# Performance work log

Measured on AMD Instinct MI355X. Metric: run time of the kernel, lower is better.

Reference implementation:

```python
import jax, jax.numpy as jnp
import numpy as np

B, LQ, D, H, NL, NP, DFF = 8, 1800, 256, 8, 4, 4, 1024
DH = D // H
SHAPES = np.array([[100, 150], [50, 75], [25, 38], [13, 19]], dtype=np.int64)
LIN = int((SHAPES[:, 0] * SHAPES[:, 1]).sum())
QN, QP = -8.0, 7.0  # 4-bit signed LSQ


def lsq(w, alpha):
    """LSQ weight quantization (per-tensor scale, STE round/grad-scale)."""
    g = 1.0 / jnp.sqrt(w.size * QP)
    a = alpha * g + jax.lax.stop_gradient(alpha - alpha * g)  # grad-scaled alpha
    wn = jnp.clip(w / a, QN, QP)
    wq = wn + jax.lax.stop_gradient(jnp.round(wn) - wn)       # round with STE
    return wq * a


def linear_q(x, w, b, a):
    return x @ lsq(w, a).T + b


def layer_norm(x, g, b, eps=1e-5):
    m = x.mean(-1, keepdims=True)
    v = ((x - m) ** 2).mean(-1, keepdims=True)
    return (x - m) / jnp.sqrt(v + eps) * g + b


def setup_inputs():
    key = jax.random.key(0)
    ks = list(jax.random.split(key, 20))

    def nrm(i, shape, s=0.02):
        return jax.random.normal(ks[i], shape, jnp.float32) * s

    def alpha(w):
        return 2.0 * jnp.mean(jnp.abs(w)) / jnp.sqrt(QP)

    qW, kW, vW, oW = nrm(0, (D, D)), nrm(1, (D, D)), nrm(2, (D, D)), nrm(3, (D, D))
    val_W = nrm(4, (D, D))
    off_W = nrm(5, (H * NL * NP * 2, D))
    aw_W = nrm(6, (H * NL * NP, D))
    out_W = nrm(7, (D, D))
    W1, W2 = nrm(8, (DFF, D)), nrm(9, (D, DFF))
    lsi = np.concatenate([[0], np.cumsum(SHAPES[:, 0] * SHAPES[:, 1])[:-1]]).astype(np.int64)
    z = jnp.zeros
    return dict(
        tgt=nrm(10, (B, LQ, D), 1.0),
        query_pos=nrm(11, (B, LQ, D), 1.0),
        reference_points=jax.random.uniform(ks[12], (B, LQ, NL, 2), jnp.float32),
        src=nrm(13, (B, LIN, D), 1.0),
        qW=qW, qb=z(D), kW=kW, kb=z(D), vW=vW, vb=z(D), oW=oW, ob=z(D),
        a_q=alpha(qW), a_k=alpha(kW), a_v=alpha(vW), a_o=alpha(oW),
        val_W=val_W, val_b=z(D), a_val=alpha(val_W),
        off_W=off_W, off_b=z(H * NL * NP * 2),
        aw_W=aw_W, aw_b=z(H * NL * NP),
        out_W=out_W, out_b=z(D), a_out=alpha(out_W),
        W1=W1, b1=z(DFF), a_w1=alpha(W1),
        W2=W2, b2=z(D), a_w2=alpha(W2),
        ln1_g=jnp.ones(D), ln1_b=z(D),
        ln2_g=jnp.ones(D), ln2_b=z(D),
        ln3_g=jnp.ones(D), ln3_b=z(D),
        src_spatial_shapes=jnp.asarray(SHAPES),
        level_start_index=jnp.asarray(lsi),
        src_padding_mask=jnp.zeros((B, LIN), dtype=bool),
    )


def reference(tgt, query_pos, reference_points, src,
              qW, qb, kW, kb, vW, vb, oW, ob, a_q, a_k, a_v, a_o,
              val_W, val_b, a_val, off_W, off_b, aw_W, aw_b, out_W, out_b, a_out,
              W1, b1, a_w1, W2, b2, a_w2,
              ln1_g, ln1_b, ln2_g, ln2_b, ln3_g, ln3_b,
              src_spatial_shapes, level_start_index, src_padding_mask):
    shapes = np.asarray(src_spatial_shapes)  # static spatial shapes per level

    # ---- quantized self-attention (dropout = eval mode, i.e. identity) ----
    qk_in = tgt + query_pos
    q = linear_q(qk_in, qW, qb, a_q).reshape(B, LQ, H, DH)
    k = linear_q(qk_in, kW, kb, a_k).reshape(B, LQ, H, DH)
    v = linear_q(tgt, vW, vb, a_v).reshape(B, LQ, H, DH)
    scores = jnp.einsum('bqhd,bkhd->bhqk', q, k) / jnp.sqrt(jnp.float32(DH))
    p = jax.nn.softmax(scores, axis=-1)
    sa = jnp.einsum('bhqk,bkhd->bqhd', p, v).reshape(B, LQ, D)
    tgt = layer_norm(tgt + linear_q(sa, oW, ob, a_o), ln2_g, ln2_b)

    # ---- quantized multi-scale deformable cross-attention ----
    query = tgt + query_pos
    value = linear_q(src, val_W, val_b, a_val)
    value = jnp.where(src_padding_mask[..., None], 0.0, value)
    value = value.reshape(B, LIN, H, DH)
    offs = (query @ off_W.T + off_b).reshape(B, LQ, H, NL, NP, 2)
    aw = (query @ aw_W.T + aw_b).reshape(B, LQ, H, NL * NP)
    aw = jax.nn.softmax(aw, axis=-1).reshape(B, LQ, H, NL, NP)
    # offset normalizer is (W_l, H_l)
    norm = jnp.asarray(shapes[:, ::-1].astype(np.float32))  # [NL, 2]
    loc = reference_points[:, :, None, :, None, :] + offs / norm[None, None, None, :, None, :]

    bidx = jnp.arange(B)[:, None, None, None]
    hidx = jnp.arange(H)[None, None, :, None]
    acc = jnp.zeros((B, LQ, H, DH), jnp.float32)
    start = 0
    for l in range(NL):
        Hl, Wl = int(shapes[l, 0]), int(shapes[l, 1])
        v_l = jax.lax.dynamic_slice_in_dim(value, start, Hl * Wl, 1).reshape(B, Hl, Wl, H, DH)
        # grid_sample semantics: align_corners=False, zero padding
        x = loc[:, :, :, l, :, 0] * Wl - 0.5  # [B, LQ, H, NP]
        y = loc[:, :, :, l, :, 1] * Hl - 0.5
        x0 = jnp.floor(x); y0 = jnp.floor(y)
        x0i = x0.astype(jnp.int32); y0i = y0.astype(jnp.int32)
        wx1 = x - x0; wy1 = y - y0
        wx0 = 1.0 - wx1; wy0 = 1.0 - wy1

        def gather(yi, xi):
            valid = (yi >= 0) & (yi < Hl) & (xi >= 0) & (xi < Wl)
            yc = jnp.clip(yi, 0, Hl - 1); xc = jnp.clip(xi, 0, Wl - 1)
            g = v_l[bidx, yc, xc, hidx]  # [B, LQ, H, NP, DH]
            return g * valid[..., None]

        samp = (gather(y0i, x0i) * (wy0 * wx0)[..., None]
                + gather(y0i, x0i + 1) * (wy0 * wx1)[..., None]
                + gather(y0i + 1, x0i) * (wy1 * wx0)[..., None]
                + gather(y0i + 1, x0i + 1) * (wy1 * wx1)[..., None])
        acc = acc + (aw[:, :, :, l, :, None] * samp).sum(axis=3)
        start += Hl * Wl

    ca = linear_q(acc.reshape(B, LQ, D), out_W, out_b, a_out)
    tgt = layer_norm(tgt + ca, ln1_g, ln1_b)

    # ---- quantized FFN ----
    t2 = linear_q(jax.nn.relu(linear_q(tgt, W1, b1, a_w1)), W2, b2, a_w2)
    tgt = layer_norm(tgt + t2, ln3_g, ln3_b)
    return tgt
```

## Files before the change

kernel.cpp:

```cpp
#include <hip/hip_runtime.h>
#include <hip/hip_bf16.h>

static constexpr int B_   = 8;
static constexpr int LQ_  = 1800;
static constexpr int D_   = 256;
static constexpr int H_   = 8;
static constexpr int DFF_ = 1024;
static constexpr int LIN_ = 19947;
static constexpr int MQ_  = B_ * LQ_;
static constexpr int NELEM_ = MQ_ * D_;

#define CDIV(a, b) (((a) + (b) - 1) / (b))

typedef unsigned short u16;
typedef unsigned int   u32;
typedef unsigned long long u64;
typedef __attribute__((ext_vector_type(8))) __bf16 bf16x8;
typedef __attribute__((ext_vector_type(4))) float  f32x4;
typedef __attribute__((ext_vector_type(4))) u32    u32x4;

#if __has_builtin(__builtin_amdgcn_exp2f)
#define EXP2(x) __builtin_amdgcn_exp2f(x)
#else
#define EXP2(x) exp2f(x)
#endif

__device__ __forceinline__ u16 f2bf(float f) {
    union { __bf16 h; u16 u; } v; v.h = (__bf16)f; return v.u;
}
__device__ __forceinline__ float bf2f(u16 u) {
    union { u32 u; float f; } v; v.u = ((u32)u) << 16;
    return v.f;
}

__device__ __forceinline__ f32x4 mfma_bf16(bf16x8 a, bf16x8 b, f32x4 c) {
    return __builtin_amdgcn_mfma_f32_16x16x32_bf16(a, b, c, 0, 0, 0);
}

__global__ void k_quant(const float* __restrict__ w, const float* __restrict__ alpha,
                        u16* __restrict__ o, int n) {
    int i = blockIdx.x * blockDim.x + threadIdx.x;
    if (i >= n) return;
    float a = alpha[0];
    float wn = fminf(fmaxf(w[i] / a, -8.f), 7.f);
    o[i] = f2bf(rintf(wn) * a);
}

__global__ void k_cvt(const float* __restrict__ w, u16* __restrict__ o, int n) {
    int i = blockIdx.x * blockDim.x + threadIdx.x;
    if (i < n) o[i] = f2bf(w[i]);
}

__global__ void k_addcvt(const float* __restrict__ a, const float* __restrict__ b,
                         u16* __restrict__ o, int n) {
    int i = blockIdx.x * blockDim.x + threadIdx.x;
    if (i < n) o[i] = f2bf(a[i] + b[i]);
}

__global__ void k_addcvt2(const u16* __restrict__ a, const float* __restrict__ b,
                          u16* __restrict__ o, int n) {
    int i = blockIdx.x * blockDim.x + threadIdx.x;
    if (i < n) o[i] = f2bf(bf2f(a[i]) + b[i]);
}

__device__ __forceinline__ bf16x8 loadx(const u16* p) { return *(const bf16x8*)p; }
__device__ __forceinline__ bf16x8 loadx(const float* p) {
    float4 a = *(const float4*)p;
    float4 b = *(const float4*)(p + 4);
    bf16x8 r;
    r[0] = (__bf16)a.x; r[1] = (__bf16)a.y; r[2] = (__bf16)a.z; r[3] = (__bf16)a.w;
    r[4] = (__bf16)b.x; r[5] = (__bf16)b.y; r[6] = (__bf16)b.z; r[7] = (__bf16)b.w;
    return r;
}
__device__ __forceinline__ void storey(float* p, float v) { *p = v; }
__device__ __forceinline__ void storey(u16* p, float v)   { *p = f2bf(v); }

template <typename XT, typename OT, bool RELU>
__global__ __launch_bounds__(256) void k_gemm(
    const XT* __restrict__ X, const u16* __restrict__ W,
    const float* __restrict__ bias, OT* __restrict__ Y,
    int M, int N, int K)
{
    __shared__ u16 As[128 * 40];
    __shared__ u16 Bs[128 * 40];
    const int tid = threadIdx.x;
    const int wave = tid >> 6, lane = tid & 63;
    const int wr = wave >> 1, wc = wave & 1;
    const int fr = lane & 15, fg = lane >> 4;
    const int bm = blockIdx.x * 128, bn = blockIdx.y * 128;
    const int srow = tid >> 2, sc = (tid & 3) * 8;

    f32x4 acc[4][4];
    #pragma unroll
    for (int m = 0; m < 4; ++m)
        #pragma unroll
        for (int n = 0; n < 4; ++n) acc[m][n] = (f32x4){0.f, 0.f, 0.f, 0.f};

    for (int k0 = 0; k0 < K; k0 += 32) {
        __syncthreads();
        #pragma unroll
        for (int i = 0; i < 2; ++i) {
            int row = srow + i * 64;
            int gr = bm + row; if (gr > M - 1) gr = M - 1;
            bf16x8 xa = loadx(X + (size_t)gr * K + k0 + sc);
            *(bf16x8*)&As[row * 40 + sc] = xa;
            bf16x8 wb = *(const bf16x8*)(W + (size_t)(bn + row) * K + k0 + sc);
            *(bf16x8*)&Bs[row * 40 + sc] = wb;
        }
        __syncthreads();
        bf16x8 af[4], bg[4];
        #pragma unroll
        for (int m = 0; m < 4; ++m)
            af[m] = *(const bf16x8*)&As[(wr * 64 + m * 16 + fr) * 40 + fg * 8];
        #pragma unroll
        for (int n = 0; n < 4; ++n)
            bg[n] = *(const bf16x8*)&Bs[(wc * 64 + n * 16 + fr) * 40 + fg * 8];
        #pragma unroll
        for (int m = 0; m < 4; ++m)
            #pragma unroll
            for (int n = 0; n < 4; ++n)
                acc[m][n] = mfma_bf16(af[m], bg[n], acc[m][n]);
    }

    #pragma unroll
    for (int m = 0; m < 4; ++m) {
        #pragma unroll
        for (int i = 0; i < 4; ++i) {
            int grow = bm + wr * 64 + m * 16 + fg * 4 + i;
            if (grow >= M) continue;
            #pragma unroll
            for (int n = 0; n < 4; ++n) {
                int gcol = bn + wc * 64 + n * 16 + fr;
                float v = acc[m][n][i] + bias[gcol];
                if (RELU) v = fmaxf(v, 0.f);
                storey(Y + (size_t)grow * N + gcol, v);
            }
        }
    }
}

__global__ __launch_bounds__(256) void k_attn(
    const u16* __restrict__ Q, const u16* __restrict__ K,
    const u16* __restrict__ V, u16* __restrict__ O)
{
    __shared__ u16 Ks[128 * 40];
    __shared__ u16 Vt[32 * 136];
    const int b = blockIdx.z, h = blockIdx.y;
    const int q0 = blockIdx.x * 64;
    const int tid = threadIdx.x;
    const int wave = tid >> 6, lane = tid & 63;
    const int fr = lane & 15, fg = lane >> 4;
    constexpr float C2 = 0.25503486f;

    int qg = q0 + wave * 16 + fr; if (qg >= LQ_) qg = LQ_ - 1;
    bf16x8 qf;
    {
        bf16x8 qraw = *(const bf16x8*)&Q[((size_t)(b * LQ_ + qg)) * 256 + h * 32 + fg * 8];
        #pragma unroll
        for (int j = 0; j < 8; ++j) qf[j] = (__bf16)((float)qraw[j] * C2);
    }

    const bf16x8 ones = {(__bf16)1.f, (__bf16)1.f, (__bf16)1.f, (__bf16)1.f,
                         (__bf16)1.f, (__bf16)1.f, (__bf16)1.f, (__bf16)1.f};

    f32x4 o0 = (f32x4){0.f,0.f,0.f,0.f}, o1 = (f32x4){0.f,0.f,0.f,0.f};
    f32x4 lacc = (f32x4){0.f,0.f,0.f,0.f};

    const int kr = tid >> 1, kc = (tid & 1) * 16;
    const int vp = lane, vdh = wave * 8;
    const int cp = ((vp >> 4) << 4) | (((vp >> 1) & 3) << 2) | (((vp >> 3) & 1) << 1) | (vp & 1);

    for (int kb0 = 0; kb0 < LQ_; kb0 += 128) {
        const bool tail = (kb0 + 128 > LQ_);
        __syncthreads();
        {
            int kg = kb0 + kr; if (kg >= LQ_) kg = LQ_ - 1;
            const u16* kp = &K[((size_t)(b * LQ_ + kg)) * 256 + h * 32 + kc];
            *(bf16x8*)&Ks[kr * 40 + kc]     = *(const bf16x8*)kp;
            *(bf16x8*)&Ks[kr * 40 + kc + 8] = *(const bf16x8*)(kp + 8);
            int v0 = kb0 + 2 * vp, v1 = v0 + 1;
            if (v0 >= LQ_) v0 = LQ_ - 1;
            if (v1 >= LQ_) v1 = LQ_ - 1;
            union { bf16x8 v; u16 s[8]; } va, vb2;
            va.v  = *(const bf16x8*)&V[((size_t)(b * LQ_ + v0)) * 256 + h * 32 + vdh];
            vb2.v = *(const bf16x8*)&V[((size_t)(b * LQ_ + v1)) * 256 + h * 32 + vdh];
            #pragma unroll
            for (int j = 0; j < 8; ++j)
                *(u32*)&Vt[(vdh + j) * 136 + 2 * cp] = (u32)va.s[j] | ((u32)vb2.s[j] << 16);
        }
        __syncthreads();

        u32x4 pq[4];
        #pragma unroll
        for (int f = 0; f < 8; ++f) {
            bf16x8 ka = *(const bf16x8*)&Ks[(f * 16 + fr) * 40 + fg * 8];
            f32x4 s = mfma_bf16(ka, qf, (f32x4){0.f,0.f,0.f,0.f});
            if (tail) {
                #pragma unroll
                for (int i = 0; i < 4; ++i)
                    if (kb0 + f * 16 + fg * 4 + i >= LQ_) s[i] = -3e38f;
            }
            float p0 = EXP2(s[0]), p1 = EXP2(s[1]);
            float p2 = EXP2(s[2]), p3 = EXP2(s[3]);
            union { __bf16 h[2]; u32 w; } c0, c1;
            c0.h[0] = (__bf16)p0; c0.h[1] = (__bf16)p1;
            c1.h[0] = (__bf16)p2; c1.h[1] = (__bf16)p3;
            pq[f >> 1][(f & 1) * 2 + 0] = c0.w;
            pq[f >> 1][(f & 1) * 2 + 1] = c1.w;
        }

        #pragma unroll
        for (int ks = 0; ks < 4; ++ks) {
            bf16x8 pb  = __builtin_bit_cast(bf16x8, pq[ks]);
            bf16x8 va0 = *(const bf16x8*)&Vt[fr * 136 + ks * 32 + fg * 8];
            bf16x8 va1 = *(const bf16x8*)&Vt[(16 + fr) * 136 + ks * 32 + fg * 8];
            o0 = mfma_bf16(va0, pb, o0);
            o1 = mfma_bf16(va1, pb, o1);
            lacc = mfma_bf16(ones, pb, lacc);
        }
    }

    float inv = 1.f / lacc[0];
    int qout = q0 + wave * 16 + fr;
    if (qout < LQ_) {
        size_t base = ((size_t)(b * LQ_ + qout)) * 256 + h * 32;
        #pragma unroll
        for (int i = 0; i < 4; ++i) {
            O[base + fg * 4 + i]      = f2bf(o0[i] * inv);
            O[base + 16 + fg * 4 + i] = f2bf(o1[i] * inv);
        }
    }
}

__device__ __forceinline__ float ldf(const float* p) { return *p; }
__device__ __forceinline__ float ldf(const u16* p)   { return bf2f(*p); }

template <typename RT, typename OT>
__global__ __launch_bounds__(256) void k_resln(
    const u16* __restrict__ X, const RT* __restrict__ R,
    const float* __restrict__ g, const float* __restrict__ bb,
    OT* __restrict__ O)
{
    const int row = blockIdx.x;
    const int d = threadIdx.x;
    const size_t off = (size_t)row * D_ + d;
    float v = ldf(R + off) + bf2f(X[off]);
    __shared__ float r1[4], r2[4];
    int lane = d & 63, wid = d >> 6;
    float s = v;
    #pragma unroll
    for (int o_ = 32; o_ >= 1; o_ >>= 1) s += __shfl_xor(s, o_);
    if (lane == 0) r1[wid] = s;
    __syncthreads();
    float mean = (r1[0] + r1[1] + r1[2] + r1[3]) * (1.f / 256.f);
    float dv = v - mean;
    float sq = dv * dv;
    #pragma unroll
    for (int o_ = 32; o_ >= 1; o_ >>= 1) sq += __shfl_xor(sq, o_);
    if (lane == 0) r2[wid] = sq;
    __syncthreads();
    float var = (r2[0] + r2[1] + r2[2] + r2[3]) * (1.f / 256.f);
    storey(O + off, dv / sqrtf(var + 1e-5f) * g[d] + bb[d]);
}

__global__ __launch_bounds__(256) void k_sample(
    const float* __restrict__ offs, const float* __restrict__ aw,
    const u16* __restrict__ value, const float* __restrict__ refp,
    u16* __restrict__ acc_out)
{
    __shared__ u32 pts[2][128][8];
    const int t = threadIdx.x;
    const int bq0 = blockIdx.x * 2;
    const int b = bq0 / LQ_;

    constexpr int Hl[4] = {100, 50, 25, 13};
    constexpr int Wl[4] = {150, 75, 38, 19};
    constexpr int LS[4] = {0, 15000, 18750, 19700};

    {
        const int qsub = t >> 7;
        const int pt = t & 127;
        const int h = pt >> 4, lp = pt & 15;
        const int l = lp >> 2, p = lp & 3;
        const int bq = bq0 + qsub;

        float2 oxy = *(const float2*)&offs[(size_t)bq * 256 + h * 32 + l * 8 + p * 2];
        float av = aw[(size_t)bq * 128 + h * 16 + lp];
        float mx = av;
        #pragma unroll
        for (int s = 1; s < 16; s <<= 1) mx = fmaxf(mx, __shfl_xor(mx, s));
        float e = __expf(av - mx);
        float sum = e;
        #pragma unroll
        for (int s = 1; s < 16; s <<= 1) sum += __shfl_xor(sum, s);
        float a = e / sum;

        float2 rxy = *(const float2*)&refp[(size_t)bq * 8 + l * 2];
        const float Wf = (float)Wl[l], Hf = (float)Hl[l];
        float x = (rxy.x + oxy.x / Wf) * Wf - 0.5f;
        float y = (rxy.y + oxy.y / Hf) * Hf - 0.5f;
        float x0f = floorf(x), y0f = floorf(y);
        int x0 = (int)x0f, y0 = (int)y0f;
        float wx1 = x - x0f, wy1 = y - y0f;
        float wx0 = 1.f - wx1, wy0 = 1.f - wy1;

        u32 ov[4]; float wv[4];
        #pragma unroll
        for (int c = 0; c < 4; ++c) {
            int cy = c >> 1, cx = c & 1;
            int yi = y0 + cy, xi = x0 + cx;
            bool valid = (yi >= 0) && (yi < Hl[l]) && (xi >= 0) && (xi < Wl[l]);
            ov[c] = valid ? (u32)((LS[l] + yi * Wl[l] + xi) * 256 + h * 32) : 0u;
            float w = (cy ? wy1 : wy0) * (cx ? wx1 : wx0) * a;
            wv[c] = valid ? w : 0.f;
        }
        u32* dst = pts[qsub][lp * 8 + h];
        *(uint4*)dst = make_uint4(ov[0], ov[1], ov[2], ov[3]);
        float4 wq = make_float4(wv[0], wv[1], wv[2], wv[3]);
        *(float4*)(dst + 4) = wq;
    }
    __syncthreads();

    const int qsub = t >> 7;
    const int h = (t >> 4) & 7;
    const int dp = t & 15;
    const u16* vb = value + (size_t)b * LIN_ * 256 + 2 * dp;
    float a0 = 0.f, a1 = 0.f;
    #pragma unroll
    for (int i = 0; i < 16; ++i) {
        const u32* P = pts[qsub][i * 8 + h];
        uint4 o4 = *(const uint4*)P;
        float4 w4 = *(const float4*)(P + 4);
        u32 g;
        g = *(const u32*)&vb[o4.x]; a0 += w4.x * bf2f((u16)g); a1 += w4.x * bf2f((u16)(g >> 16));
        g = *(const u32*)&vb[o4.y]; a0 += w4.y * bf2f((u16)g); a1 += w4.y * bf2f((u16)(g >> 16));
        g = *(const u32*)&vb[o4.z]; a0 += w4.z * bf2f((u16)g); a1 += w4.z * bf2f((u16)(g >> 16));
        g = *(const u32*)&vb[o4.w]; a0 += w4.w * bf2f((u16)g); a1 += w4.w * bf2f((u16)(g >> 16));
    }
    const int bq = bq0 + qsub;
    u32 packed = (u32)f2bf(a0) | ((u32)f2bf(a1) << 16);
    *(u32*)&acc_out[(size_t)bq * 256 + h * 32 + 2 * dp] = packed;
}

extern "C" void kernel_launch(void* const* d_in, const int* in_sizes, int n_in,
                              void* d_out, int out_size, void* d_ws, size_t ws_size,
                              hipStream_t stream)
{
    (void)in_sizes; (void)n_in; (void)out_size; (void)ws_size;
    const float* tgt   = (const float*)d_in[0];
    const float* qpos  = (const float*)d_in[1];
    const float* refp  = (const float*)d_in[2];
    const float* src   = (const float*)d_in[3];
    const float* qW    = (const float*)d_in[4];
    const float* qb    = (const float*)d_in[5];
    const float* kW    = (const float*)d_in[6];
    const float* kb    = (const float*)d_in[7];
    const float* vW    = (const float*)d_in[8];
    const float* vb    = (const float*)d_in[9];
    const float* oW    = (const float*)d_in[10];
    const float* ob    = (const float*)d_in[11];
    const float* a_q   = (const float*)d_in[12];
    const float* a_k   = (const float*)d_in[13];
    const float* a_v   = (const float*)d_in[14];
    const float* a_o   = (const float*)d_in[15];
    const float* val_W = (const float*)d_in[16];
    const float* val_b = (const float*)d_in[17];
    const float* a_val = (const float*)d_in[18];
    const float* off_W = (const float*)d_in[19];
    const float* off_b = (const float*)d_in[20];
    const float* aw_W  = (const float*)d_in[21];
    const float* aw_b  = (const float*)d_in[22];
    const float* out_W = (const float*)d_in[23];
    const float* out_b = (const float*)d_in[24];
    const float* a_out = (const float*)d_in[25];
    const float* W1    = (const float*)d_in[26];
    const float* b1    = (const float*)d_in[27];
    const float* a_w1  = (const float*)d_in[28];
    const float* W2    = (const float*)d_in[29];
    const float* b2    = (const float*)d_in[30];
    const float* a_w2  = (const float*)d_in[31];
    const float* ln1_g = (const float*)d_in[32];
    const float* ln1_b = (const float*)d_in[33];
    const float* ln2_g = (const float*)d_in[34];
    const float* ln2_b = (const float*)d_in[35];
    const float* ln3_g = (const float*)d_in[36];
    const float* ln3_b = (const float*)d_in[37];

    u16* wq_q  = (u16*)d_ws;
    u16* wq_k  = wq_q + 65536;
    u16* wq_v  = wq_k + 65536;
    u16* wq_o  = wq_v + 65536;
    u16* wq_vl = wq_o + 65536;
    u16* wq_ot = wq_vl + 65536;
    u16* w_off = wq_ot + 65536;
    u16* w_aw  = w_off + 65536;
    u16* wq_1  = w_aw + 32768;
    u16* wq_2  = wq_1 + 262144;
    u16* bufA  = wq_2 + 262144;
    u16* bufB  = bufA + NELEM_;
    u16* bufC  = bufB + NELEM_;
    u16* bufD  = bufC + NELEM_;
    u16* bufE  = bufD + NELEM_;
    float* offs = (float*)(bufE + NELEM_);
    float* awb  = offs + NELEM_;
    u16* valb   = (u16*)(awb + MQ_ * 128);

    const int TB = 256;
    const int MVAL = B_ * LIN_;

    k_quant<<<CDIV(65536, TB), TB, 0, stream>>>(qW, a_q, wq_q, 65536);
    k_quant<<<CDIV(65536, TB), TB, 0, stream>>>(kW, a_k, wq_k, 65536);
    k_quant<<<CDIV(65536, TB), TB, 0, stream>>>(vW, a_v, wq_v, 65536);
    k_quant<<<CDIV(65536, TB), TB, 0, stream>>>(oW, a_o, wq_o, 65536);
    k_quant<<<CDIV(65536, TB), TB, 0, stream>>>(val_W, a_val, wq_vl, 65536);
    k_quant<<<CDIV(65536, TB), TB, 0, stream>>>(out_W, a_out, wq_ot, 65536);
    k_quant<<<CDIV(262144, TB), TB, 0, stream>>>(W1, a_w1, wq_1, 262144);
    k_quant<<<CDIV(262144, TB), TB, 0, stream>>>(W2, a_w2, wq_2, 262144);
    k_cvt<<<CDIV(65536, TB), TB, 0, stream>>>(off_W, w_off, 65536);
    k_cvt<<<CDIV(32768, TB), TB, 0, stream>>>(aw_W, w_aw, 32768);

    k_addcvt<<<CDIV(NELEM_, TB), TB, 0, stream>>>(tgt, qpos, bufA, NELEM_);
    k_cvt<<<CDIV(NELEM_, TB), TB, 0, stream>>>(tgt, bufB, NELEM_);

    k_gemm<u16, u16, false><<<dim3(CDIV(MQ_,128), 2), TB, 0, stream>>>(bufA, wq_q, qb, bufC, MQ_, 256, 256);
    k_gemm<u16, u16, false><<<dim3(CDIV(MQ_,128), 2), TB, 0, stream>>>(bufA, wq_k, kb, bufD, MQ_, 256, 256);
    k_gemm<u16, u16, false><<<dim3(CDIV(MQ_,128), 2), TB, 0, stream>>>(bufB, wq_v, vb, bufE, MQ_, 256, 256);
    k_attn<<<dim3(CDIV(LQ_,64), H_, B_), TB, 0, stream>>>(bufC, bufD, bufE, bufA);
    k_gemm<u16, u16, false><<<dim3(CDIV(MQ_,128), 2), TB, 0, stream>>>(bufA, wq_o, ob, bufB, MQ_, 256, 256);
    k_resln<float, u16><<<MQ_, TB, 0, stream>>>(bufB, tgt, ln2_g, ln2_b, bufC);

    k_addcvt2<<<CDIV(NELEM_, TB), TB, 0, stream>>>(bufC, qpos, bufD, NELEM_);
    k_gemm<float, u16, false><<<dim3(CDIV(MVAL,128), 2), TB, 0, stream>>>(src, wq_vl, val_b, valb, MVAL, 256, 256);
    k_gemm<u16, float, false><<<dim3(CDIV(MQ_,128), 2), TB, 0, stream>>>(bufD, w_off, off_b, offs, MQ_, 256, 256);
    k_gemm<u16, float, false><<<dim3(CDIV(MQ_,128), 1), TB, 0, stream>>>(bufD, w_aw, aw_b, awb, MQ_, 128, 256);
    k_sample<<<MQ_ / 2, TB, 0, stream>>>(offs, awb, valb, refp, bufE);
    k_gemm<u16, u16, false><<<dim3(CDIV(MQ_,128), 2), TB, 0, stream>>>(bufE, wq_ot, out_b, bufA, MQ_, 256, 256);
    k_resln<u16, u16><<<MQ_, TB, 0, stream>>>(bufA, bufC, ln1_g, ln1_b, bufB);

    u16* ffn1 = valb;
    k_gemm<u16, u16, true ><<<dim3(CDIV(MQ_,128), 8), TB, 0, stream>>>(bufB, wq_1, b1, ffn1, MQ_, 1024, 256);
    k_gemm<u16, u16, false><<<dim3(CDIV(MQ_,128), 2), TB, 0, stream>>>(ffn1, wq_2, b2, bufD, MQ_, 256, 1024);
    k_resln<u16, float><<<MQ_, TB, 0, stream>>>(bufD, bufB, ln3_g, ln3_b, (float*)d_out);
}
```

Before: 416.5 us.

## Add double-buffered 128x256 GEMM kernel with register prefetch for projection GEMMs

Adds a new GEMM kernel using 512 threads and a 128x256 output tile, so each block covers the full N=256 width and the A tile is loaded once instead of twice. The LDS tiles are double-buffered and the next K-slice is prefetched into registers while MFMAs run on the current one, which removes one barrier per iteration and overlaps global loads with compute. All 256-wide and FFN GEMMs are switched to it; the old kernel gains N-bound guards and stays for the 128-wide attention-weight GEMM. Larger tiles mean fewer blocks per launch and more registers and LDS per block, which may lower occupancy.

```diff
diff --git a/kernel.cpp b/kernel.cpp
--- a/kernel.cpp
+++ b/kernel.cpp
@@ -63,26 +63,112 @@
     if (i < n) o[i] = f2bf(bf2f(a[i]) + b[i]);
 }
 
-__device__ __forceinline__ bf16x8 loadx(const u16* p) { return *(const bf16x8*)p; }
-__device__ __forceinline__ bf16x8 loadx(const float* p) {
-    float4 a = *(const float4*)p;
-    float4 b = *(const float4*)(p + 4);
+struct rawf8 { float4 a, b; };
+__device__ __forceinline__ bf16x8 loadraw(const u16* p) { return *(const bf16x8*)p; }
+__device__ __forceinline__ rawf8  loadraw(const float* p) {
+    rawf8 r; r.a = *(const float4*)p; r.b = *(const float4*)(p + 4); return r;
+}
+__device__ __forceinline__ void wlds(u16* d, bf16x8 v) { *(bf16x8*)d = v; }
+__device__ __forceinline__ void wlds(u16* d, rawf8 v) {
     bf16x8 r;
-    r[0] = (__bf16)a.x; r[1] = (__bf16)a.y; r[2] = (__bf16)a.z; r[3] = (__bf16)a.w;
-    r[4] = (__bf16)b.x; r[5] = (__bf16)b.y; r[6] = (__bf16)b.z; r[7] = (__bf16)b.w;
-    return r;
+    r[0] = (__bf16)v.a.x; r[1] = (__bf16)v.a.y; r[2] = (__bf16)v.a.z; r[3] = (__bf16)v.a.w;
+    r[4] = (__bf16)v.b.x; r[5] = (__bf16)v.b.y; r[6] = (__bf16)v.b.z; r[7] = (__bf16)v.b.w;
+    *(bf16x8*)d = r;
 }
 __device__ __forceinline__ void storey(float* p, float v) { *p = v; }
 __device__ __forceinline__ void storey(u16* p, float v)   { *p = f2bf(v); }
 
+template <typename XT, typename OT, bool RELU>
+__global__ __launch_bounds__(512) void k_gemm2(
+    const XT* __restrict__ X, const u16* __restrict__ W,
+    const float* __restrict__ bias, OT* __restrict__ Y,
+    int M, int N, int K)
+{
+    __shared__ u16 As[2][128 * 40];
+    __shared__ u16 Bs[2][256 * 40];
+    const int tid = threadIdx.x;
+    const int wave = tid >> 6, lane = tid & 63;
+    const int wr = wave >> 2, wc = wave & 3;
+    const int fr = lane & 15, fg = lane >> 4;
+    const int bm = blockIdx.x * 128, bn = blockIdx.y * 256;
+
+    const int xr = tid >> 2, xc = (tid & 3) * 8;
+    const int wrow = tid >> 1, wcol = (tid & 1) * 16;
+
+    int gr0 = bm + xr; if (gr0 > M - 1) gr0 = M - 1;
+    const XT*  xp0 = X + (size_t)gr0 * K + xc;
+    const u16* wp0 = W + (size_t)(bn + wrow) * K + wcol;
+
+    f32x4 acc[4][4];
+    #pragma unroll
+    for (int m = 0; m < 4; ++m)
+        #pragma unroll
+        for (int n = 0; n < 4; ++n) acc[m][n] = (f32x4){0.f, 0.f, 0.f, 0.f};
+
+    wlds(&As[0][xr * 40 + xc], loadraw(xp0));
+    wlds(&Bs[0][wrow * 40 + wcol],     loadraw(wp0));
+    wlds(&Bs[0][wrow * 40 + wcol + 8], loadraw(wp0 + 8));
+    __syncthreads();
+
+    const int nk = K >> 5;
+    int cur = 0;
+    for (int kt = 0; kt < nk; ++kt) {
+        const bool nxt = (kt + 1 < nk);
+        decltype(loadraw(xp0)) xa{};
+        bf16x8 wb0{}, wb1{};
+        if (nxt) {
+            int k0 = (kt + 1) << 5;
+            xa  = loadraw(xp0 + k0);
+            wb0 = loadraw(wp0 + k0);
+            wb1 = loadraw(wp0 + k0 + 8);
+        }
+        bf16x8 af[4], bg[4];
+        #pragma unroll
+        for (int m = 0; m < 4; ++m)
+            af[m] = *(const bf16x8*)&As[cur][(wr * 64 + m * 16 + fr) * 40 + fg * 8];
+        #pragma unroll
+        for (int n = 0; n < 4; ++n)
+            bg[n] = *(const bf16x8*)&Bs[cur][(wc * 64 + n * 16 + fr) * 40 + fg * 8];
+        #pragma unroll
+        for (int m = 0; m < 4; ++m)
+            #pragma unroll
+            for (int n = 0; n < 4; ++n)
+                acc[m][n] = mfma_bf16(af[m], bg[n], acc[m][n]);
+        if (nxt) {
+            wlds(&As[cur ^ 1][xr * 40 + xc], xa);
+            wlds(&Bs[cur ^ 1][wrow * 40 + wcol],     wb0);
+            wlds(&Bs[cur ^ 1][wrow * 40 + wcol + 8], wb1);
+            __syncthreads();
+            cur ^= 1;
+        }
+    }
+
+    #pragma unroll
+    for (int m = 0; m < 4; ++m) {
+        #pragma unroll
+        for (int i = 0; i < 4; ++i) {
+            int grow = bm + wr * 64 + m * 16 + fg * 4 + i;
+            if (grow >= M) continue;
+            #pragma unroll
+            for (int n = 0; n < 4; ++n) {
+                int gcol = bn + wc * 64 + n * 16 + fr;
+                float v = acc[m][n][i] + bias[gcol];
+                if (RELU) v = fmaxf(v, 0.f);
+                storey(Y + (size_t)grow * N + gcol, v);
+            }
+        }
+    }
+}
+
+__device__ __forceinline__ bf16x8 loadx(const u16* p) { return *(const bf16x8*)p; }
 template <typename XT, typename OT, bool RELU>
 __global__ __launch_bounds__(256) void k_gemm(
     const XT* __restrict__ X, const u16* __restrict__ W,
     const float* __restrict__ bias, OT* __restrict__ Y,
     int M, int N, int K)
 {
-    __shared__ u16 As[128 * 40];
-    __shared__ u16 Bs[128 * 40];
+    __shared__ u16 Ash[128 * 40];
+    __shared__ u16 Bsh[128 * 40];
     const int tid = threadIdx.x;
     const int wave = tid >> 6, lane = tid & 63;
     const int wr = wave >> 1, wc = wave & 1;
@@ -102,19 +188,18 @@
         for (int i = 0; i < 2; ++i) {
             int row = srow + i * 64;
             int gr = bm + row; if (gr > M - 1) gr = M - 1;
-            bf16x8 xa = loadx(X + (size_t)gr * K + k0 + sc);
-            *(bf16x8*)&As[row * 40 + sc] = xa;
-            bf16x8 wb = *(const bf16x8*)(W + (size_t)(bn + row) * K + k0 + sc);
-            *(bf16x8*)&Bs[row * 40 + sc] = wb;
+            wlds(&Ash[row * 40 + sc], loadraw(X + (size_t)gr * K + k0 + sc));
+            int wn = bn + row; if (wn > N - 1) wn = N - 1;
+            wlds(&Bsh[row * 40 + sc], loadraw(W + (size_t)wn * K + k0 + sc));
         }
         __syncthreads();
         bf16x8 af[4], bg[4];
         #pragma unroll
         for (int m = 0; m < 4; ++m)
-            af[m] = *(const bf16x8*)&As[(wr * 64 + m * 16 + fr) * 40 + fg * 8];
+            af[m] = *(const bf16x8*)&Ash[(wr * 64 + m * 16 + fr) * 40 + fg * 8];
         #pragma unroll
         for (int n = 0; n < 4; ++n)
-            bg[n] = *(const bf16x8*)&Bs[(wc * 64 + n * 16 + fr) * 40 + fg * 8];
+            bg[n] = *(const bf16x8*)&Bsh[(wc * 64 + n * 16 + fr) * 40 + fg * 8];
         #pragma unroll
         for (int m = 0; m < 4; ++m)
             #pragma unroll
@@ -131,6 +216,7 @@
             #pragma unroll
             for (int n = 0; n < 4; ++n) {
                 int gcol = bn + wc * 64 + n * 16 + fr;
+                if (gcol >= N) continue;
                 float v = acc[m][n][i] + bias[gcol];
                 if (RELU) v = fmaxf(v, 0.f);
                 storey(Y + (size_t)grow * N + gcol, v);
@@ -407,6 +493,7 @@
 
     const int TB = 256;
     const int MVAL = B_ * LIN_;
+    const int GX = CDIV(MQ_, 128);
 
     k_quant<<<CDIV(65536, TB), TB, 0, stream>>>(qW, a_q, wq_q, 65536);
     k_quant<<<CDIV(65536, TB), TB, 0, stream>>>(kW, a_k, wq_k, 65536);
@@ -422,23 +509,23 @@
     k_addcvt<<<CDIV(NELEM_, TB), TB, 0, stream>>>(tgt, qpos, bufA, NELEM_);
     k_cvt<<<CDIV(NELEM_, TB), TB, 0, stream>>>(tgt, bufB, NELEM_);
 
-    k_gemm<u16, u16, false><<<dim3(CDIV(MQ_,128), 2), TB, 0, stream>>>(bufA, wq_q, qb, bufC, MQ_, 256, 256);
-    k_gemm<u16, u16, false><<<dim3(CDIV(MQ_,128), 2), TB, 0, stream>>>(bufA, wq_k, kb, bufD, MQ_, 256, 256);
-    k_gemm<u16, u16, false><<<dim3(CDIV(MQ_,128), 2), TB, 0, stream>>>(bufB, wq_v, vb, bufE, MQ_, 256, 256);
+    k_gemm2<u16, u16, false><<<dim3(GX, 1), 512, 0, stream>>>(bufA, wq_q, qb, bufC, MQ_, 256, 256);
+    k_gemm2<u16, u16, false><<<dim3(GX, 1), 512, 0, stream>>>(bufA, wq_k, kb, bufD, MQ_, 256, 256);
+    k_gemm2<u16, u16, false><<<dim3(GX, 1), 512, 0, stream>>>(bufB, wq_v, vb, bufE, MQ_, 256, 256);
     k_attn<<<dim3(CDIV(LQ_,64), H_, B_), TB, 0, stream>>>(bufC, bufD, bufE, bufA);
-    k_gemm<u16, u16, false><<<dim3(CDIV(MQ_,128), 2), TB, 0, stream>>>(bufA, wq_o, ob, bufB, MQ_, 256, 256);
+    k_gemm2<u16, u16, false><<<dim3(GX, 1), 512, 0, stream>>>(bufA, wq_o, ob, bufB, MQ_, 256, 256);
     k_resln<float, u16><<<MQ_, TB, 0, stream>>>(bufB, tgt, ln2_g, ln2_b, bufC);
 
     k_addcvt2<<<CDIV(NELEM_, TB), TB, 0, stream>>>(bufC, qpos, bufD, NELEM_);
-    k_gemm<float, u16, false><<<dim3(CDIV(MVAL,128), 2), TB, 0, stream>>>(src, wq_vl, val_b, valb, MVAL, 256, 256);
-    k_gemm<u16, float, false><<<dim3(CDIV(MQ_,128), 2), TB, 0, stream>>>(bufD, w_off, off_b, offs, MQ_, 256, 256);
-    k_gemm<u16, float, false><<<dim3(CDIV(MQ_,128), 1), TB, 0, stream>>>(bufD, w_aw, aw_b, awb, MQ_, 128, 256);
+    k_gemm2<float, u16, false><<<dim3(CDIV(MVAL,128), 1), 512, 0, stream>>>(src, wq_vl, val_b, valb, MVAL, 256, 256);
+    k_gemm2<u16, float, false><<<dim3(GX, 1), 512, 0, stream>>>(bufD, w_off, off_b, offs, MQ_, 256, 256);
+    k_gemm<u16, float, false><<<dim3(GX, 1), TB, 0, stream>>>(bufD, w_aw, aw_b, awb, MQ_, 128, 256);
     k_sample<<<MQ_ / 2, TB, 0, stream>>>(offs, awb, valb, refp, bufE);
-    k_gemm<u16, u16, false><<<dim3(CDIV(MQ_,128), 2), TB, 0, stream>>>(bufE, wq_ot, out_b, bufA, MQ_, 256, 256);
+    k_gemm2<u16, u16, false><<<dim3(GX, 1), 512, 0, stream>>>(bufE, wq_ot, out_b, bufA, MQ_, 256, 256);
     k_resln<u16, u16><<<MQ_, TB, 0, stream>>>(bufA, bufC, ln1_g, ln1_b, bufB);
 
     u16* ffn1 = valb;
-    k_gemm<u16, u16, true ><<<dim3(CDIV(MQ_,128), 8), TB, 0, stream>>>(bufB, wq_1, b1, ffn1, MQ_, 1024, 256);
-    k_gemm<u16, u16, false><<<dim3(CDIV(MQ_,128), 2), TB, 0, stream>>>(ffn1, wq_2, b2, bufD, MQ_, 256, 1024);
+    k_gemm2<u16, u16, true ><<<dim3(GX, 4), 512, 0, stream>>>(bufB, wq_1, b1, ffn1, MQ_, 1024, 256);
+    k_gemm2<u16, u16, false><<<dim3(GX, 1), 512, 0, stream>>>(ffn1, wq_2, b2, bufD, MQ_, 256, 1024);
     k_resln<u16, float><<<MQ_, TB, 0, stream>>>(bufD, bufB, ln3_g, ln3_b, (float*)d_out);
 }
```

New measurement: 398.6 us. 1.05x faster.
